# Performance work log

Measured on AMD Instinct MI355X. Metric: run time of the kernel, lower is better.

Reference implementation:

```python
import jax, jax.numpy as jnp
import numpy as np

N_USERS = 50000
N_ITEMS = 50000
N_NODES = N_USERS + N_ITEMS
EMB = 64
N_LAYERS = 3
N_EDGES = 1_600_000
BATCH = 16384
REG = 1e-5
SLOPE = 0.01  # F.leaky_relu default negative_slope
EPS = 1e-12   # F.normalize default eps


def setup_inputs() -> dict:
    key = jax.random.key(0)
    ks = jax.random.split(key, 12)
    u = jax.random.randint(ks[0], (BATCH,), 0, N_USERS)
    i = jax.random.randint(ks[1], (BATCH,), 0, N_ITEMS)
    j = jax.random.randint(ks[2], (BATCH,), 0, N_ITEMS)
    rows = jax.random.randint(ks[3], (N_EDGES,), 0, N_NODES)
    cols = jax.random.randint(ks[4], (N_EDGES,), 0, N_NODES)
    # values of the symmetric-normalized adjacency (small positive)
    vals = jax.random.uniform(ks[5], (N_EDGES,), dtype=jnp.float32) * 0.05
    # xavier-uniform-like init for embeddings and weights
    u_emb = jax.random.normal(ks[6], (N_USERS, EMB), dtype=jnp.float32) * 0.1
    i_emb = jax.random.normal(ks[7], (N_ITEMS, EMB), dtype=jnp.float32) * 0.1
    scale = 1.0 / np.sqrt(EMB)
    W1_w = jax.random.normal(ks[8], (N_LAYERS, EMB, EMB), dtype=jnp.float32) * scale
    W1_b = jnp.zeros((N_LAYERS, EMB), dtype=jnp.float32)
    W2_w = jax.random.normal(ks[9], (N_LAYERS, EMB, EMB), dtype=jnp.float32) * scale
    W2_b = jnp.zeros((N_LAYERS, EMB), dtype=jnp.float32)
    return {"u": u, "i": i, "j": j, "rows": rows, "cols": cols, "vals": vals,
            "u_emb": u_emb, "i_emb": i_emb,
            "W1_w": W1_w, "W1_b": W1_b, "W2_w": W2_w, "W2_b": W2_b}


def reference(u, i, j, rows, cols, vals, u_emb, i_emb, W1_w, W1_b, W2_w, W2_b):
    # ego embeddings over all nodes: [N, D]
    ego = jnp.concatenate([u_emb, i_emb], axis=0)
    preds = [ego]
    for k in range(N_LAYERS):
        # SpMM over COO edges (fold concatenation == full SpMM):
        # ws[r] = sum_e vals[e] * ego[cols[e]] for rows[e] == r
        msgs = vals[:, None] * ego[cols]                       # [E, D]
        ws = jax.ops.segment_sum(msgs, rows, num_segments=N_NODES)  # [N, D]
        aff = ego * ws                                         # elementwise affinity
        # torch Linear: x @ W.T + b
        t = ws @ W1_w[k].T + W1_b[k] + aff @ W2_w[k].T + W2_b[k]
        ego = jnp.where(t >= 0, t, SLOPE * t)                  # leaky_relu (mess_dropout=0)
        norm = ego / jnp.maximum(
            jnp.linalg.norm(ego, axis=1, keepdims=True), EPS)  # F.normalize(p=2, dim=1)
        preds.append(norm)
    pred = jnp.concatenate(preds, axis=1)                      # [N, EMB*(1+L)]
    u_g, i_g = pred[:N_USERS], pred[N_USERS:]
    u_e, p_e, n_e = u_g[u], i_g[i], i_g[j]
    y_ui = jnp.sum(u_e * p_e, axis=1)
    y_uj = jnp.sum(u_e * n_e, axis=1)
    log_prob = jnp.mean(jax.nn.log_sigmoid(y_ui - y_uj))
    bpr_loss = -log_prob
    l2 = (jnp.sum(u_e ** 2) / 2.0 + jnp.sum(p_e ** 2) / 2.0
          + jnp.sum(n_e ** 2) / 2.0) / u_e.shape[0]
    return bpr_loss + REG * l2
```

## Files before the change

### kernel.cpp

```cpp
#include <hip/hip_runtime.h>
#include <math.h>

#define N_USERS 50000
#define N_ITEMS 50000
#define N_NODES 100000
#define N_NODES_PAD 100032
#define EMB 64
#define N_LAYERS 3
#define N_EDGES 1600000
#define BATCH 16384
#define REG_C 1e-05f
#define SLOPE 0.01f
#define EPS_C 1e-12f

#define NBUK 391
#define TILE_C 6144
#define SPK_MAX 4608

#define VAL_ENC 655360.0f
#define VAL_DEC (1.0f / 655360.0f)

typedef __attribute__((ext_vector_type(8))) short bf16x8;
typedef __attribute__((ext_vector_type(4))) float f32x4;

__device__ __forceinline__ unsigned short f2bf(float f) {
    unsigned int b = __float_as_uint(f);
    return (unsigned short)((b + 0x7fffu + ((b >> 16) & 1u)) >> 16);
}
__device__ __forceinline__ unsigned int pack2bf(float a, float b) {
    return (unsigned int)f2bf(a) | ((unsigned int)f2bf(b) << 16);
}

__global__ void k_init_ego(const float* __restrict__ u_emb,
                           const float* __restrict__ i_emb,
                           float* __restrict__ ego,
                           unsigned short* __restrict__ ego_bf) {
    int idx = blockIdx.x * blockDim.x + threadIdx.x;
    const int n4 = N_NODES * EMB / 4;
    if (idx < n4) {
        const int u4 = N_USERS * EMB / 4;
        float4 v = (idx < u4) ? ((const float4*)u_emb)[idx]
                              : ((const float4*)i_emb)[idx - u4];
        ((float4*)ego)[idx] = v;
        ushort4 h;
        h.x = f2bf(v.x); h.y = f2bf(v.y); h.z = f2bf(v.z); h.w = f2bf(v.w);
        *(ushort4*)&ego_bf[(size_t)idx * 4] = h;
    }
}

__global__ __launch_bounds__(256) void k_buk_histo(const int* __restrict__ rows,
                                                   int* __restrict__ bukhist) {
    __shared__ int h[NBUK];
    for (int i = threadIdx.x; i < NBUK; i += 256) h[i] = 0;
    __syncthreads();
    int stride = gridDim.x * blockDim.x;
    for (int e = blockIdx.x * blockDim.x + threadIdx.x; e < N_EDGES; e += stride)
        atomicAdd(&h[rows[e] >> 8], 1);
    __syncthreads();
    for (int i = threadIdx.x; i < NBUK; i += 256)
        if (h[i]) atomicAdd(&bukhist[i], h[i]);
}

__global__ __launch_bounds__(512) void k_buk_scan(const int* __restrict__ bukhist,
                                                  int* __restrict__ bukbase,
                                                  int* __restrict__ bukcur) {
    __shared__ int s[512];
    int t = threadIdx.x;
    int v = (t < NBUK) ? bukhist[t] : 0;
    s[t] = v;
    __syncthreads();
    for (int st = 1; st < 512; st <<= 1) {
        int a = (t >= st) ? s[t - st] : 0;
        __syncthreads();
        s[t] += a;
        __syncthreads();
    }
    if (t < NBUK) { bukbase[t] = s[t] - v; bukcur[t] = s[t] - v; }
    if (t == 0) bukbase[NBUK] = N_EDGES;
}

__global__ __launch_bounds__(512) void k_bucket_scatter(const int* __restrict__ rows,
                                                        const int* __restrict__ cols,
                                                        const float* __restrict__ vals,
                                                        int* __restrict__ bukcur,
                                                        uint2* __restrict__ bucketed) {
    __shared__ uint2 stage[TILE_C];
    __shared__ int hist[NBUK];
    __shared__ int lofs[NBUK];
    __shared__ int lcur[NBUK];
    __shared__ int gbase[NBUK];
    __shared__ int scan_s[512];
    int tid = threadIdx.x;
    int e0 = blockIdx.x * TILE_C;
    int n = min(TILE_C, N_EDGES - e0);

    for (int i = tid; i < NBUK; i += 512) hist[i] = 0;
    __syncthreads();
    for (int i = tid; i < n; i += 512) atomicAdd(&hist[rows[e0 + i] >> 8], 1);
    __syncthreads();
    int v = (tid < NBUK) ? hist[tid] : 0;
    scan_s[tid] = v;
    __syncthreads();
    for (int st = 1; st < 512; st <<= 1) {
        int a = (tid >= st) ? scan_s[tid - st] : 0;
        __syncthreads();
        scan_s[tid] += a;
        __syncthreads();
    }
    if (tid < NBUK) {
        int excl = scan_s[tid] - v;
        lofs[tid] = excl;
        lcur[tid] = excl;
        gbase[tid] = v ? atomicAdd(&bukcur[tid], v) : 0;
    }
    __syncthreads();
    for (int i = tid; i < n; i += 512) {
        int e = e0 + i;
        int r = rows[e];
        unsigned int q = __float2uint_rn(vals[e] * VAL_ENC);
        q = (q > 32767u) ? 32767u : q;
        unsigned int pk = (unsigned int)cols[e] | (q << 17);
        int pos = atomicAdd(&lcur[r >> 8], 1);
        stage[pos] = make_uint2(pk, (unsigned int)r);
    }
    __syncthreads();
    for (int i = tid; i < n; i += 512) {
        uint2 w = stage[i];
        int b = w.y >> 8;
        bucketed[gbase[b] + (i - lofs[b])] = w;
    }
}

__global__ __launch_bounds__(256) void k_bucket_sort(const int* __restrict__ bukbase,
                                                     const uint2* __restrict__ bucketed,
                                                     unsigned int* __restrict__ edge_pk,
                                                     int* __restrict__ offsets) {
    __shared__ int hist[256];
    __shared__ int lofs[256];
    __shared__ int lcur[256];
    __shared__ unsigned int spk[SPK_MAX];
    int b = blockIdx.x, tid = threadIdx.x;
    int s = bukbase[b], e = bukbase[b + 1];
    int cnt = e - s;
    int r0 = b << 8;
    int nrows = min(256, N_NODES - r0);

    hist[tid] = 0;
    __syncthreads();
    for (int i = tid; i < cnt; i += 256) atomicAdd(&hist[bucketed[s + i].y & 255u], 1);
    __syncthreads();
    int v = hist[tid];
    lofs[tid] = v;
    __syncthreads();
    for (int st = 1; st < 256; st <<= 1) {
        int a = (tid >= st) ? lofs[tid - st] : 0;
        __syncthreads();
        lofs[tid] += a;
        __syncthreads();
    }
    int excl = lofs[tid] - v;
    __syncthreads();
    lofs[tid] = excl;
    lcur[tid] = excl;
    if (tid < nrows) offsets[r0 + tid] = s + excl;
    if (b == NBUK - 1 && tid == 0) offsets[N_NODES] = N_EDGES;
    __syncthreads();

    if (cnt <= SPK_MAX) {
        for (int i = tid; i < cnt; i += 256) {
            uint2 w = bucketed[s + i];
            int p = atomicAdd(&lcur[w.y & 255u], 1);
            spk[p] = w.x;
        }
        __syncthreads();
        for (int i = tid; i < cnt; i += 256) edge_pk[s + i] = spk[i];
    } else {
        for (int i = tid; i < cnt; i += 256) {
            uint2 w = bucketed[s + i];
            int p = atomicAdd(&lcur[w.y & 255u], 1);
            edge_pk[s + p] = w.x;
        }
    }
}

__global__ __launch_bounds__(256) void k_edge_agg(const int* __restrict__ offsets,
                                                  const unsigned int* __restrict__ edge_pk,
                                                  const unsigned short* __restrict__ ego_bf,
                                                  float* __restrict__ wsacc) {
    int wid = blockIdx.x * 4 + (threadIdx.x >> 6);
    int lane = threadIdx.x & 63;
    int half = lane >> 5;
    int g = (lane >> 3) & 3;
    int h = lane & 7;
    int n = wid * 2 + half;
    if (n >= N_NODES) return;
    int o0 = offsets[n], o1 = offsets[n + 1];
    int d = o1 - o0;
    int T = (d + 3) >> 2;
    float a0 = 0.f, a1 = 0.f, a2 = 0.f, a3 = 0.f;
    float a4 = 0.f, a5 = 0.f, a6 = 0.f, a7 = 0.f;
    int e = o0 + g;
    unsigned int pk = (e < o1) ? edge_pk[e] : 0u;
    for (int t = 0; t < T; ++t) {
        unsigned int cur = pk;
        int en = e + 4;
        pk = (en < o1) ? edge_pk[en] : 0u;
        int c = (int)(cur & 0x1FFFFu);
        float v = (float)(cur >> 17) * VAL_DEC;
        uint4 r = *(const uint4*)&ego_bf[(size_t)c * EMB + h * 8];
        a0 += v * __uint_as_float(r.x << 16);
        a1 += v * __uint_as_float(r.x & 0xffff0000u);
        a2 += v * __uint_as_float(r.y << 16);
        a3 += v * __uint_as_float(r.y & 0xffff0000u);
        a4 += v * __uint_as_float(r.z << 16);
        a5 += v * __uint_as_float(r.z & 0xffff0000u);
        a6 += v * __uint_as_float(r.w << 16);
        a7 += v * __uint_as_float(r.w & 0xffff0000u);
        e = en;
    }
    a0 += __shfl_xor(a0, 8, 64);  a1 += __shfl_xor(a1, 8, 64);
    a2 += __shfl_xor(a2, 8, 64);  a3 += __shfl_xor(a3, 8, 64);
    a4 += __shfl_xor(a4, 8, 64);  a5 += __shfl_xor(a5, 8, 64);
    a6 += __shfl_xor(a6, 8, 64);  a7 += __shfl_xor(a7, 8, 64);
    a0 += __shfl_xor(a0, 16, 64); a1 += __shfl_xor(a1, 16, 64);
    a2 += __shfl_xor(a2, 16, 64); a3 += __shfl_xor(a3, 16, 64);
    a4 += __shfl_xor(a4, 16, 64); a5 += __shfl_xor(a5, 16, 64);
    a6 += __shfl_xor(a6, 16, 64); a7 += __shfl_xor(a7, 16, 64);
    if (g == 0) {
        size_t base = (size_t)n * EMB + h * 8;
        *(float4*)&wsacc[base]     = make_float4(a0, a1, a2, a3);
        *(float4*)&wsacc[base + 4] = make_float4(a4, a5, a6, a7);
    }
}

__global__ __launch_bounds__(256) void k_transform(const float* __restrict__ wsacc,
                                                   float* __restrict__ ego,
                                                   unsigned short* __restrict__ ego_bf,
                                                   const float* __restrict__ W1,
                                                   const float* __restrict__ b1,
                                                   const float* __restrict__ W2,
                                                   const float* __restrict__ b2) {
    __shared__ short Xs16[64 * 128];
    __shared__ short Wb[16 * 64 * 8];
    int tid = threadIdx.x;
    int r0 = blockIdx.x * 64;

    for (int u = tid; u < 1024; u += 256) {
        int fidx = u >> 6, ln = u & 63;
        int s = fidx >> 2, j = fidx & 3;
        int c = j * 16 + (ln & 15);
        int k = s * 32 + ((ln >> 4) << 3);
        const float* Wsrc = (k < 64) ? &W1[c * 64 + k] : &W2[c * 64 + (k - 64)];
        float4 wlo = *(const float4*)Wsrc;
        float4 whi = *(const float4*)(Wsrc + 4);
        uint4 o;
        o.x = pack2bf(wlo.x, wlo.y); o.y = pack2bf(wlo.z, wlo.w);
        o.z = pack2bf(whi.x, whi.y); o.w = pack2bf(whi.z, whi.w);
        *(uint4*)&Wb[u * 8] = o;
    }

    for (int u = tid; u < 1024; u += 256) {
        int row = u >> 4, kc = u & 15;
        size_t gbase = (size_t)(r0 + row) * EMB + ((kc & 7) << 3);
        float4 wlo = *(const float4*)&wsacc[gbase];
        float4 whi = *(const float4*)&wsacc[gbase + 4];
        float f0 = wlo.x, f1 = wlo.y, f2 = wlo.z, f3 = wlo.w;
        float f4 = whi.x, f5 = whi.y, f6 = whi.z, f7 = whi.w;
        if (kc >= 8) {
            uint4 eb = *(const uint4*)&ego_bf[gbase];
            f0 *= __uint_as_float(eb.x << 16);
            f1 *= __uint_as_float(eb.x & 0xffff0000u);
            f2 *= __uint_as_float(eb.y << 16);
            f3 *= __uint_as_float(eb.y & 0xffff0000u);
            f4 *= __uint_as_float(eb.z << 16);
            f5 *= __uint_as_float(eb.z & 0xffff0000u);
            f6 *= __uint_as_float(eb.w << 16);
            f7 *= __uint_as_float(eb.w & 0xffff0000u);
        }
        uint4 o;
        o.x = pack2bf(f0, f1); o.y = pack2bf(f2, f3);
        o.z = pack2bf(f4, f5); o.w = pack2bf(f6, f7);
        *(uint4*)&Xs16[(row * 16 + (kc ^ (row & 7))) * 8] = o;
    }
    __syncthreads();

    int l = tid & 63, wv = tid >> 6;
    int arow = wv * 16 + (l & 15);
    f32x4 acc[4];
    #pragma unroll
    for (int j = 0; j < 4; ++j) acc[j] = (f32x4){0.f, 0.f, 0.f, 0.f};
    #pragma unroll
    for (int s = 0; s < 4; ++s) {
        bf16x8 af = *(const bf16x8*)&Xs16[(arow * 16 + ((s * 4 + (l >> 4)) ^ (l & 7))) * 8];
        #pragma unroll
        for (int j = 0; j < 4; ++j) {
            bf16x8 bfr = *(const bf16x8*)&Wb[((s * 4 + j) * 64 + l) * 8];
            acc[j] = __builtin_amdgcn_mfma_f32_16x16x32_bf16(af, bfr, acc[j], 0, 0, 0);
        }
    }

    int orow = r0 + wv * 16 + ((l >> 4) << 2);
    int ocol = l & 15;
    #pragma unroll
    for (int j = 0; j < 4; ++j) {
        int col = j * 16 + ocol;
        float bias = b1[col] + b2[col];
        #pragma unroll
        for (int r = 0; r < 4; ++r) {
            float t = acc[j][r] + bias;
            float o = (t >= 0.f) ? t : SLOPE * t;
            size_t g = (size_t)(orow + r) * EMB + col;
            ego[g] = o;
            ego_bf[g] = f2bf(o);
        }
    }
}

__global__ __launch_bounds__(256) void k_batch_acc(const float* __restrict__ src,
                                                   const int* __restrict__ u,
                                                   const int* __restrict__ ii,
                                                   const int* __restrict__ jj,
                                                   float* __restrict__ acc,
                                                   int normalize) {
    int wid = (blockIdx.x * blockDim.x + threadIdx.x) >> 6;
    int lane = threadIdx.x & 63;
    if (wid >= BATCH) return;
    int nu = u[wid];
    int np_ = N_USERS + ii[wid];
    int nn = N_USERS + jj[wid];
    float eu = src[(size_t)nu * EMB + lane];
    float ep = src[(size_t)np_ * EMB + lane];
    float en = src[(size_t)nn * EMB + lane];
    float d_up = eu * ep, d_un = eu * en;
    float s_u = eu * eu, s_p = ep * ep, s_n = en * en;
    #pragma unroll
    for (int m = 32; m > 0; m >>= 1) {
        d_up += __shfl_xor(d_up, m, 64);
        d_un += __shfl_xor(d_un, m, 64);
        s_u  += __shfl_xor(s_u,  m, 64);
        s_p  += __shfl_xor(s_p,  m, 64);
        s_n  += __shfl_xor(s_n,  m, 64);
    }
    if (lane == 0) {
        if (normalize) {
            float inu = 1.f / fmaxf(sqrtf(s_u), EPS_C);
            float inp = 1.f / fmaxf(sqrtf(s_p), EPS_C);
            float inn = 1.f / fmaxf(sqrtf(s_n), EPS_C);
            d_up *= inu * inp;
            d_un *= inu * inn;
            s_u *= inu * inu;
            s_p *= inp * inp;
            s_n *= inn * inn;
        }
        acc[0 * BATCH + wid] += d_up;
        acc[1 * BATCH + wid] += d_un;
        acc[2 * BATCH + wid] += s_u;
        acc[3 * BATCH + wid] += s_p;
        acc[4 * BATCH + wid] += s_n;
    }
}

__global__ __launch_bounds__(1024) void k_finalize(const float* __restrict__ acc,
                                                   float* __restrict__ out) {
    __shared__ float s1[1024], s2[1024];
    float ls = 0.f, l2 = 0.f;
    for (int b = threadIdx.x; b < BATCH; b += 1024) {
        float x = acc[0 * BATCH + b] - acc[1 * BATCH + b];
        ls += fminf(x, 0.f) - log1pf(expf(-fabsf(x)));
        l2 += acc[2 * BATCH + b] + acc[3 * BATCH + b] + acc[4 * BATCH + b];
    }
    s1[threadIdx.x] = ls; s2[threadIdx.x] = l2;
    __syncthreads();
    for (int st = 512; st > 0; st >>= 1) {
        if ((int)threadIdx.x < st) {
            s1[threadIdx.x] += s1[threadIdx.x + st];
            s2[threadIdx.x] += s2[threadIdx.x + st];
        }
        __syncthreads();
    }
    if (threadIdx.x == 0)
        out[0] = -s1[0] / (float)BATCH + REG_C * (s2[0] * 0.5f) / (float)BATCH;
}

extern "C" void kernel_launch(void* const* d_in, const int* in_sizes, int n_in,
                              void* d_out, int out_size, void* d_ws, size_t ws_size,
                              hipStream_t stream) {
    (void)in_sizes; (void)n_in; (void)out_size; (void)ws_size;
    const int*   u     = (const int*)d_in[0];
    const int*   ii    = (const int*)d_in[1];
    const int*   jj    = (const int*)d_in[2];
    const int*   rows  = (const int*)d_in[3];
    const int*   cols  = (const int*)d_in[4];
    const float* vals  = (const float*)d_in[5];
    const float* u_emb = (const float*)d_in[6];
    const float* i_emb = (const float*)d_in[7];
    const float* W1_w  = (const float*)d_in[8];
    const float* W1_b  = (const float*)d_in[9];
    const float* W2_w  = (const float*)d_in[10];
    const float* W2_b  = (const float*)d_in[11];
    float* out = (float*)d_out;

    char* p = (char*)d_ws;
    float*          ego     = (float*)p;          p += (size_t)N_NODES_PAD * EMB * 4;
    float*          wsacc   = (float*)p;          p += (size_t)N_NODES_PAD * EMB * 4;
    unsigned short* ego_bf  = (unsigned short*)p; p += (size_t)N_NODES_PAD * EMB * 2;
    unsigned int*   edge_pk = (unsigned int*)p;   p += (size_t)N_EDGES * 4;
    int*   offsets  = (int*)p;    p += (size_t)(N_NODES + 1) * 4;
    int*   bukhist  = (int*)p;    p += (size_t)NBUK * 4;
    int*   bukbase  = (int*)p;    p += (size_t)(NBUK + 1) * 4;
    int*   bukcur   = (int*)p;    p += (size_t)NBUK * 4;
    float* acc      = (float*)p;  p += (size_t)5 * BATCH * 4;
    uint2* bucketed = (uint2*)wsacc;

    hipMemsetAsync(bukhist, 0, (size_t)NBUK * 4, stream);
    hipMemsetAsync(acc, 0, (size_t)5 * BATCH * 4, stream);

    k_init_ego<<<(N_NODES * EMB / 4 + 255) / 256, 256, 0, stream>>>(u_emb, i_emb, ego, ego_bf);
    k_buk_histo<<<256, 256, 0, stream>>>(rows, bukhist);
    k_buk_scan<<<1, 512, 0, stream>>>(bukhist, bukbase, bukcur);
    k_bucket_scatter<<<(N_EDGES + TILE_C - 1) / TILE_C, 512, 0, stream>>>(rows, cols, vals, bukcur, bucketed);
    k_bucket_sort<<<NBUK, 256, 0, stream>>>(bukbase, bucketed, edge_pk, offsets);

    k_batch_acc<<<BATCH * 64 / 256, 256, 0, stream>>>(ego, u, ii, jj, acc, 0);

    for (int k = 0; k < N_LAYERS; ++k) {
        k_edge_agg<<<(N_NODES / 2 + 3) / 4, 256, 0, stream>>>(offsets, edge_pk, ego_bf, wsacc);
        k_transform<<<(N_NODES + 63) / 64, 256, 0, stream>>>(wsacc, ego, ego_bf,
                                              W1_w + k * 4096, W1_b + k * 64,
                                              W2_w + k * 4096, W2_b + k * 64);
        k_batch_acc<<<BATCH * 64 / 256, 256, 0, stream>>>(ego, u, ii, jj, acc, 1);
    }
    k_finalize<<<1, 1024, 0, stream>>>(acc, out);
}
```

Measured before the change: 285.9 us.

## Fuse edge aggregation into layer transform kernel and drop fp32 ego copy

Merges the SpMM gather kernel into the MFMA transform kernel, so each block aggregates its 64 rows directly into shared memory as bf16 instead of writing and rereading a fp32 wsacc buffer. The fp32 ego array is removed: layers ping-pong between two bf16 buffers, and the batch scorer reads bf16. This saves global traffic and kernel launches. In exchange the layer kernel has fewer waves doing irregular gathers per block, which could reduce latency hiding. Batch scoring now also runs on bf16 values, which lowers precision.

```diff
diff --git a/kernel.cpp b/kernel.cpp
--- a/kernel.cpp
+++ b/kernel.cpp
@@ -30,10 +30,12 @@
 __device__ __forceinline__ unsigned int pack2bf(float a, float b) {
     return (unsigned int)f2bf(a) | ((unsigned int)f2bf(b) << 16);
 }
+__device__ __forceinline__ float bf2f(unsigned short v) {
+    return __uint_as_float(((unsigned int)v) << 16);
+}
 
 __global__ void k_init_ego(const float* __restrict__ u_emb,
                            const float* __restrict__ i_emb,
-                           float* __restrict__ ego,
                            unsigned short* __restrict__ ego_bf) {
     int idx = blockIdx.x * blockDim.x + threadIdx.x;
     const int n4 = N_NODES * EMB / 4;
@@ -41,7 +43,6 @@
         const int u4 = N_USERS * EMB / 4;
         float4 v = (idx < u4) ? ((const float4*)u_emb)[idx]
                               : ((const float4*)i_emb)[idx - u4];
-        ((float4*)ego)[idx] = v;
         ushort4 h;
         h.x = f2bf(v.x); h.y = f2bf(v.y); h.z = f2bf(v.z); h.w = f2bf(v.w);
         *(ushort4*)&ego_bf[(size_t)idx * 4] = h;
@@ -183,67 +184,19 @@
     }
 }
 
-__global__ __launch_bounds__(256) void k_edge_agg(const int* __restrict__ offsets,
-                                                  const unsigned int* __restrict__ edge_pk,
-                                                  const unsigned short* __restrict__ ego_bf,
-                                                  float* __restrict__ wsacc) {
-    int wid = blockIdx.x * 4 + (threadIdx.x >> 6);
-    int lane = threadIdx.x & 63;
-    int half = lane >> 5;
-    int g = (lane >> 3) & 3;
-    int h = lane & 7;
-    int n = wid * 2 + half;
-    if (n >= N_NODES) return;
-    int o0 = offsets[n], o1 = offsets[n + 1];
-    int d = o1 - o0;
-    int T = (d + 3) >> 2;
-    float a0 = 0.f, a1 = 0.f, a2 = 0.f, a3 = 0.f;
-    float a4 = 0.f, a5 = 0.f, a6 = 0.f, a7 = 0.f;
-    int e = o0 + g;
-    unsigned int pk = (e < o1) ? edge_pk[e] : 0u;
-    for (int t = 0; t < T; ++t) {
-        unsigned int cur = pk;
-        int en = e + 4;
-        pk = (en < o1) ? edge_pk[en] : 0u;
-        int c = (int)(cur & 0x1FFFFu);
-        float v = (float)(cur >> 17) * VAL_DEC;
-        uint4 r = *(const uint4*)&ego_bf[(size_t)c * EMB + h * 8];
-        a0 += v * __uint_as_float(r.x << 16);
-        a1 += v * __uint_as_float(r.x & 0xffff0000u);
-        a2 += v * __uint_as_float(r.y << 16);
-        a3 += v * __uint_as_float(r.y & 0xffff0000u);
-        a4 += v * __uint_as_float(r.z << 16);
-        a5 += v * __uint_as_float(r.z & 0xffff0000u);
-        a6 += v * __uint_as_float(r.w << 16);
-        a7 += v * __uint_as_float(r.w & 0xffff0000u);
-        e = en;
-    }
-    a0 += __shfl_xor(a0, 8, 64);  a1 += __shfl_xor(a1, 8, 64);
-    a2 += __shfl_xor(a2, 8, 64);  a3 += __shfl_xor(a3, 8, 64);
-    a4 += __shfl_xor(a4, 8, 64);  a5 += __shfl_xor(a5, 8, 64);
-    a6 += __shfl_xor(a6, 8, 64);  a7 += __shfl_xor(a7, 8, 64);
-    a0 += __shfl_xor(a0, 16, 64); a1 += __shfl_xor(a1, 16, 64);
-    a2 += __shfl_xor(a2, 16, 64); a3 += __shfl_xor(a3, 16, 64);
-    a4 += __shfl_xor(a4, 16, 64); a5 += __shfl_xor(a5, 16, 64);
-    a6 += __shfl_xor(a6, 16, 64); a7 += __shfl_xor(a7, 16, 64);
-    if (g == 0) {
-        size_t base = (size_t)n * EMB + h * 8;
-        *(float4*)&wsacc[base]     = make_float4(a0, a1, a2, a3);
-        *(float4*)&wsacc[base + 4] = make_float4(a4, a5, a6, a7);
-    }
-}
-
-__global__ __launch_bounds__(256) void k_transform(const float* __restrict__ wsacc,
-                                                   float* __restrict__ ego,
-                                                   unsigned short* __restrict__ ego_bf,
-                                                   const float* __restrict__ W1,
-                                                   const float* __restrict__ b1,
-                                                   const float* __restrict__ W2,
-                                                   const float* __restrict__ b2) {
+__global__ __launch_bounds__(256) void k_layer(const int* __restrict__ offsets,
+                                               const unsigned int* __restrict__ edge_pk,
+                                               const unsigned short* __restrict__ ego_in,
+                                               unsigned short* __restrict__ ego_out,
+                                               const float* __restrict__ W1,
+                                               const float* __restrict__ b1,
+                                               const float* __restrict__ W2,
+                                               const float* __restrict__ b2) {
     __shared__ short Xs16[64 * 128];
     __shared__ short Wb[16 * 64 * 8];
     int tid = threadIdx.x;
     int r0 = blockIdx.x * 64;
+    int l = tid & 63, wv = tid >> 6;
 
     for (int u = tid; u < 1024; u += 256) {
         int fidx = u >> 6, ln = u & 63;
@@ -259,32 +212,71 @@
         *(uint4*)&Wb[u * 8] = o;
     }
 
-    for (int u = tid; u < 1024; u += 256) {
-        int row = u >> 4, kc = u & 15;
-        size_t gbase = (size_t)(r0 + row) * EMB + ((kc & 7) << 3);
-        float4 wlo = *(const float4*)&wsacc[gbase];
-        float4 whi = *(const float4*)&wsacc[gbase + 4];
-        float f0 = wlo.x, f1 = wlo.y, f2 = wlo.z, f3 = wlo.w;
-        float f4 = whi.x, f5 = whi.y, f6 = whi.z, f7 = whi.w;
-        if (kc >= 8) {
-            uint4 eb = *(const uint4*)&ego_bf[gbase];
-            f0 *= __uint_as_float(eb.x << 16);
-            f1 *= __uint_as_float(eb.x & 0xffff0000u);
-            f2 *= __uint_as_float(eb.y << 16);
-            f3 *= __uint_as_float(eb.y & 0xffff0000u);
-            f4 *= __uint_as_float(eb.z << 16);
-            f5 *= __uint_as_float(eb.z & 0xffff0000u);
-            f6 *= __uint_as_float(eb.w << 16);
-            f7 *= __uint_as_float(eb.w & 0xffff0000u);
-        }
-        uint4 o;
-        o.x = pack2bf(f0, f1); o.y = pack2bf(f2, f3);
-        o.z = pack2bf(f4, f5); o.w = pack2bf(f6, f7);
-        *(uint4*)&Xs16[(row * 16 + (kc ^ (row & 7))) * 8] = o;
-    }
-    __syncthreads();
-
-    int l = tid & 63, wv = tid >> 6;
+    int half = l >> 5;
+    int g = (l >> 3) & 3;
+    int h = l & 7;
+    for (int p = 0; p < 8; ++p) {
+        int row = wv * 16 + p * 2 + half;
+        int n = r0 + row;
+        float a0 = 0.f, a1 = 0.f, a2 = 0.f, a3 = 0.f;
+        float a4 = 0.f, a5 = 0.f, a6 = 0.f, a7 = 0.f;
+        if (n < N_NODES) {
+            int o0 = offsets[n], o1 = offsets[n + 1];
+            int T = (o1 - o0 + 3) >> 2;
+            int e = o0 + g;
+            unsigned int pk = (e < o1) ? edge_pk[e] : 0u;
+            for (int t = 0; t < T; ++t) {
+                unsigned int cur = pk;
+                int en = e + 4;
+                pk = (en < o1) ? edge_pk[en] : 0u;
+                int c = (int)(cur & 0x1FFFFu);
+                float v = (float)(cur >> 17) * VAL_DEC;
+                uint4 r = *(const uint4*)&ego_in[(size_t)c * EMB + h * 8];
+                a0 += v * __uint_as_float(r.x << 16);
+                a1 += v * __uint_as_float(r.x & 0xffff0000u);
+                a2 += v * __uint_as_float(r.y << 16);
+                a3 += v * __uint_as_float(r.y & 0xffff0000u);
+                a4 += v * __uint_as_float(r.z << 16);
+                a5 += v * __uint_as_float(r.z & 0xffff0000u);
+                a6 += v * __uint_as_float(r.w << 16);
+                a7 += v * __uint_as_float(r.w & 0xffff0000u);
+                e = en;
+            }
+        }
+        a0 += __shfl_xor(a0, 8, 64);  a1 += __shfl_xor(a1, 8, 64);
+        a2 += __shfl_xor(a2, 8, 64);  a3 += __shfl_xor(a3, 8, 64);
+        a4 += __shfl_xor(a4, 8, 64);  a5 += __shfl_xor(a5, 8, 64);
+        a6 += __shfl_xor(a6, 8, 64);  a7 += __shfl_xor(a7, 8, 64);
+        a0 += __shfl_xor(a0, 16, 64); a1 += __shfl_xor(a1, 16, 64);
+        a2 += __shfl_xor(a2, 16, 64); a3 += __shfl_xor(a3, 16, 64);
+        a4 += __shfl_xor(a4, 16, 64); a5 += __shfl_xor(a5, 16, 64);
+        a6 += __shfl_xor(a6, 16, 64); a7 += __shfl_xor(a7, 16, 64);
+        if (g == 0) {
+            float e0 = 0.f, e1 = 0.f, e2 = 0.f, e3 = 0.f;
+            float e4 = 0.f, e5 = 0.f, e6 = 0.f, e7 = 0.f;
+            if (n < N_NODES) {
+                uint4 eb = *(const uint4*)&ego_in[(size_t)n * EMB + h * 8];
+                e0 = __uint_as_float(eb.x << 16);
+                e1 = __uint_as_float(eb.x & 0xffff0000u);
+                e2 = __uint_as_float(eb.y << 16);
+                e3 = __uint_as_float(eb.y & 0xffff0000u);
+                e4 = __uint_as_float(eb.z << 16);
+                e5 = __uint_as_float(eb.z & 0xffff0000u);
+                e6 = __uint_as_float(eb.w << 16);
+                e7 = __uint_as_float(eb.w & 0xffff0000u);
+            }
+            uint4 wsp, afp;
+            wsp.x = pack2bf(a0, a1);           wsp.y = pack2bf(a2, a3);
+            wsp.z = pack2bf(a4, a5);           wsp.w = pack2bf(a6, a7);
+            afp.x = pack2bf(a0 * e0, a1 * e1); afp.y = pack2bf(a2 * e2, a3 * e3);
+            afp.z = pack2bf(a4 * e4, a5 * e5); afp.w = pack2bf(a6 * e6, a7 * e7);
+            int sw = row & 7;
+            *(uint4*)&Xs16[(row * 16 + (h ^ sw)) * 8]       = wsp;
+            *(uint4*)&Xs16[(row * 16 + ((8 + h) ^ sw)) * 8] = afp;
+        }
+    }
+    __syncthreads();
+
     int arow = wv * 16 + (l & 15);
     f32x4 acc[4];
     #pragma unroll
@@ -309,14 +301,12 @@
         for (int r = 0; r < 4; ++r) {
             float t = acc[j][r] + bias;
             float o = (t >= 0.f) ? t : SLOPE * t;
-            size_t g = (size_t)(orow + r) * EMB + col;
-            ego[g] = o;
-            ego_bf[g] = f2bf(o);
-        }
-    }
-}
-
-__global__ __launch_bounds__(256) void k_batch_acc(const float* __restrict__ src,
+            ego_out[(size_t)(orow + r) * EMB + col] = f2bf(o);
+        }
+    }
+}
+
+__global__ __launch_bounds__(256) void k_batch_acc(const unsigned short* __restrict__ src,
                                                    const int* __restrict__ u,
                                                    const int* __restrict__ ii,
                                                    const int* __restrict__ jj,
@@ -328,9 +318,9 @@
     int nu = u[wid];
     int np_ = N_USERS + ii[wid];
     int nn = N_USERS + jj[wid];
-    float eu = src[(size_t)nu * EMB + lane];
-    float ep = src[(size_t)np_ * EMB + lane];
-    float en = src[(size_t)nn * EMB + lane];
+    float eu = bf2f(src[(size_t)nu * EMB + lane]);
+    float ep = bf2f(src[(size_t)np_ * EMB + lane]);
+    float en = bf2f(src[(size_t)nn * EMB + lane]);
     float d_up = eu * ep, d_un = eu * en;
     float s_u = eu * eu, s_p = ep * ep, s_n = en * en;
     #pragma unroll
@@ -401,34 +391,35 @@
     float* out = (float*)d_out;
 
     char* p = (char*)d_ws;
-    float*          ego     = (float*)p;          p += (size_t)N_NODES_PAD * EMB * 4;
-    float*          wsacc   = (float*)p;          p += (size_t)N_NODES_PAD * EMB * 4;
-    unsigned short* ego_bf  = (unsigned short*)p; p += (size_t)N_NODES_PAD * EMB * 2;
+    unsigned short* egoA    = (unsigned short*)p; p += (size_t)N_NODES_PAD * EMB * 2;
+    unsigned short* egoB    = (unsigned short*)p; p += (size_t)N_NODES_PAD * EMB * 2;
+    uint2*          bucketed= (uint2*)p;          p += (size_t)N_EDGES * 8;
     unsigned int*   edge_pk = (unsigned int*)p;   p += (size_t)N_EDGES * 4;
     int*   offsets  = (int*)p;    p += (size_t)(N_NODES + 1) * 4;
     int*   bukhist  = (int*)p;    p += (size_t)NBUK * 4;
     int*   bukbase  = (int*)p;    p += (size_t)(NBUK + 1) * 4;
     int*   bukcur   = (int*)p;    p += (size_t)NBUK * 4;
     float* acc      = (float*)p;  p += (size_t)5 * BATCH * 4;
-    uint2* bucketed = (uint2*)wsacc;
 
     hipMemsetAsync(bukhist, 0, (size_t)NBUK * 4, stream);
     hipMemsetAsync(acc, 0, (size_t)5 * BATCH * 4, stream);
 
-    k_init_ego<<<(N_NODES * EMB / 4 + 255) / 256, 256, 0, stream>>>(u_emb, i_emb, ego, ego_bf);
+    k_init_ego<<<(N_NODES * EMB / 4 + 255) / 256, 256, 0, stream>>>(u_emb, i_emb, egoA);
     k_buk_histo<<<256, 256, 0, stream>>>(rows, bukhist);
     k_buk_scan<<<1, 512, 0, stream>>>(bukhist, bukbase, bukcur);
     k_bucket_scatter<<<(N_EDGES + TILE_C - 1) / TILE_C, 512, 0, stream>>>(rows, cols, vals, bukcur, bucketed);
     k_bucket_sort<<<NBUK, 256, 0, stream>>>(bukbase, bucketed, edge_pk, offsets);
 
-    k_batch_acc<<<BATCH * 64 / 256, 256, 0, stream>>>(ego, u, ii, jj, acc, 0);
-
+    k_batch_acc<<<BATCH * 64 / 256, 256, 0, stream>>>(egoA, u, ii, jj, acc, 0);
+
+    unsigned short* src = egoA;
+    unsigned short* dst = egoB;
     for (int k = 0; k < N_LAYERS; ++k) {
-        k_edge_agg<<<(N_NODES / 2 + 3) / 4, 256, 0, stream>>>(offsets, edge_pk, ego_bf, wsacc);
-        k_transform<<<(N_NODES + 63) / 64, 256, 0, stream>>>(wsacc, ego, ego_bf,
+        k_layer<<<(N_NODES + 63) / 64, 256, 0, stream>>>(offsets, edge_pk, src, dst,
                                               W1_w + k * 4096, W1_b + k * 64,
                                               W2_w + k * 4096, W2_b + k * 64);
-        k_batch_acc<<<BATCH * 64 / 256, 256, 0, stream>>>(ego, u, ii, jj, acc, 1);
+        k_batch_acc<<<BATCH * 64 / 256, 256, 0, stream>>>(dst, u, ii, jj, acc, 1);
+        unsigned short* tmp = src; src = dst; dst = tmp;
     }
     k_finalize<<<1, 1024, 0, stream>>>(acc, out);
 }
```

Result: slower. 350.1 us (+22.5%).
